# Performance work log

Measured on AMD Instinct MI355X. Metric: run time of the kernel, lower is better.

The kernel has to match this reference:

```python
import jax, jax.numpy as jnp
import numpy as np

TOP_K = 2

def setup_inputs() -> dict:
    key = jax.random.key(0)
    k0, k1, k2, k3 = jax.random.split(key, 4)
    B, T, D, F, E = 2, 2048, 1024, 4096, 8
    x = jax.random.normal(k0, (B, T, D), dtype=jnp.float32)
    Wr = jax.random.normal(k1, (E, D), dtype=jnp.float32) * 0.02   # router weight [out=E, in=D]
    W1 = jax.random.normal(k2, (E, F, D), dtype=jnp.float32) * 0.02  # per-expert up-proj [out=F, in=D]
    W2 = jax.random.normal(k3, (E, D, F), dtype=jnp.float32) * 0.02  # per-expert down-proj [out=D, in=F]
    return {"x": x, "Wr": Wr, "W1": W1, "W2": W2}

def reference(x, Wr, W1, W2):
    B, T, D = x.shape
    E = Wr.shape[0]
    N = B * T
    xf = x.reshape(N, D)
    # Router in fp32 on the un-cast activations (as in the torch module).
    logits = xf @ Wr.T                                   # [N, E]
    probs = jax.nn.softmax(logits, axis=-1)
    topk_w, topk_idx = jax.lax.top_k(probs, TOP_K)       # [N, K]
    topk_w = topk_w / jnp.sum(topk_w, axis=-1, keepdims=True)
    # Combine weights scattered into a dense [N, E] dispatch/combine matrix
    # (top_k indices are distinct, so .set is exact).
    combine = jnp.zeros((N, E), dtype=jnp.float32)
    combine = combine.at[jnp.arange(N)[:, None], topk_idx].set(topk_w)
    # Expert FFN runs in bf16 (comm_dtype in the original all-to-all pipeline).
    xb = xf.astype(jnp.bfloat16)
    h = jax.nn.gelu(jnp.einsum('nd,efd->enf', xb, W1.astype(jnp.bfloat16)),
                    approximate=False)                   # [E, N, F]
    yo = jnp.einsum('enf,edf->end', h, W2.astype(jnp.bfloat16))  # [E, N, D]
    # Weighted combine: bf16 expert outputs * fp32 gate weights -> fp32 (torch promotion).
    out = jnp.einsum('end,ne->nd', yo.astype(jnp.float32), combine)
    return out.reshape(B, T, D)
```

## Files before the change

### kernel.cpp

```cpp
#include <hip/hip_runtime.h>
#include <hip/hip_bf16.h>

typedef __attribute__((ext_vector_type(8))) __bf16 bf16x8;
typedef __attribute__((ext_vector_type(4))) float floatx4;

constexpr int N_TOK = 4096;
constexpr int DDIM  = 1024;
constexpr int FDIM  = 4096;
constexpr int NEXP  = 8;
constexpr int NSLOT = 2 * N_TOK;

static __device__ __forceinline__ unsigned short f2bf(float f) {
    union { __hip_bfloat16 h; unsigned short u; } v;
    v.h = __float2bfloat16(f);
    return v.u;
}

static __device__ __forceinline__ void gl2lds16(const unsigned short* g, unsigned short* l) {
    __builtin_amdgcn_global_load_lds(
        (__attribute__((address_space(1))) void*)g,
        (__attribute__((address_space(3))) void*)l,
        16, 0, 0);
}

__global__ void castX_kernel(const float* __restrict__ src, unsigned short* __restrict__ dst,
                             int* __restrict__ counts) {
    int i = blockIdx.x * 256 + threadIdx.x;
    float4 v = *(const float4*)(src + (size_t)i * 4);
    ushort4 o;
    o.x = f2bf(v.x); o.y = f2bf(v.y); o.z = f2bf(v.z); o.w = f2bf(v.w);
    *(ushort4*)(dst + (size_t)i * 4) = o;
    if (blockIdx.x == 0 && threadIdx.x < NEXP) counts[threadIdx.x] = 0;
}

__global__ void castN_kernel(const float* __restrict__ src, unsigned short* __restrict__ dst, int n4) {
    int i = blockIdx.x * 256 + threadIdx.x;
    if (i >= n4) return;
    float4 v = *(const float4*)(src + (size_t)i * 4);
    ushort4 o;
    o.x = f2bf(v.x); o.y = f2bf(v.y); o.z = f2bf(v.z); o.w = f2bf(v.w);
    *(ushort4*)(dst + (size_t)i * 4) = o;
}

__global__ void router_kernel(const float* __restrict__ x, const float* __restrict__ Wr,
                              int* __restrict__ te, float* __restrict__ tw,
                              int* __restrict__ counts) {
    __shared__ float wr[NEXP * DDIM];
    const int tid = threadIdx.x;
    for (int i = tid; i < NEXP * DDIM; i += 256) wr[i] = Wr[i];
    __syncthreads();
    const int wave = tid >> 6, lane = tid & 63;
    const int t = blockIdx.x * 4 + wave;

    float xr[16];
    const float* xp = x + (size_t)t * DDIM;
    #pragma unroll
    for (int i = 0; i < 16; i++) xr[i] = xp[lane + 64 * i];

    float logit[NEXP];
    #pragma unroll
    for (int e = 0; e < NEXP; e++) {
        float s = 0.f;
        #pragma unroll
        for (int i = 0; i < 16; i++) s += xr[i] * wr[e * DDIM + lane + 64 * i];
        #pragma unroll
        for (int off = 32; off > 0; off >>= 1) s += __shfl_xor(s, off, 64);
        logit[e] = s;
    }
    if (lane == 0) {
        int i0 = 0; float l0 = logit[0];
        #pragma unroll
        for (int e = 1; e < NEXP; e++) if (logit[e] > l0) { l0 = logit[e]; i0 = e; }
        int i1 = -1; float l1 = -3.0e38f;
        #pragma unroll
        for (int e = 0; e < NEXP; e++) if (e != i0 && logit[e] > l1) { l1 = logit[e]; i1 = e; }
        float p1 = expf(l1 - l0);
        float w0 = 1.f / (1.f + p1);
        float w1 = p1 * w0;
        te[t * 2] = i0; te[t * 2 + 1] = i1;
        tw[t * 2] = w0; tw[t * 2 + 1] = w1;
        atomicAdd(&counts[i0], 1);
        atomicAdd(&counts[i1], 1);
    }
}

__global__ void scan_kernel(const int* __restrict__ counts, int* __restrict__ offsets,
                            int* __restrict__ cursors) {
    if (threadIdx.x == 0) {
        int acc = 0;
        for (int e = 0; e < NEXP; e++) { offsets[e] = acc; acc += counts[e]; }
        offsets[NEXP] = acc;
    }
    if (threadIdx.x < NEXP) cursors[threadIdx.x] = 0;
}

__global__ void scatter_kernel(const int* __restrict__ te, const float* __restrict__ tw,
                               const int* __restrict__ offsets, int* __restrict__ cursors,
                               int* __restrict__ rowid, float* __restrict__ gate,
                               int* __restrict__ tok2slot) {
    int t = blockIdx.x * 256 + threadIdx.x;
    if (t >= N_TOK) return;
    #pragma unroll
    for (int k = 0; k < 2; k++) {
        int e = te[t * 2 + k];
        int pos = atomicAdd(&cursors[e], 1);
        int slot = offsets[e] + pos;
        rowid[slot] = t;
        gate[slot] = tw[t * 2 + k];
        tok2slot[t * 2 + k] = slot;
    }
}

template <int K, bool UP, bool BF16W>
__global__ __launch_bounds__(256)
void ffn_gemm(const unsigned short* __restrict__ A,
              const float* __restrict__ Wf,
              const unsigned short* __restrict__ Wb,
              unsigned short* __restrict__ Hout,
              float* __restrict__ Y,
              const int* __restrict__ rowid,
              const float* __restrict__ gate,
              const int* __restrict__ offsets) {
    constexpr int BM = 128, BN = 128, BK = 32, LDT = 32;
    constexpr int NOUT = UP ? FDIM : DDIM;

    const int e = blockIdx.z;
    const int seg = offsets[e];
    const int cnt = offsets[e + 1] - seg;
    const int m0 = blockIdx.y * BM;
    if (m0 >= cnt) return;
    const int n0 = blockIdx.x * BN;

    __shared__ __align__(16) unsigned short As[BM * LDT];
    __shared__ __align__(16) unsigned short Bs[BN * LDT];

    const int tid = threadIdx.x;
    const int lane = tid & 63;
    const int wave = tid >> 6;

    const int srow0 = wave * 32 + (lane >> 2);
    const int chunk = lane & 3;

    const unsigned short* ag[2];
    #pragma unroll
    for (int j = 0; j < 2; j++) {
        int r = srow0 + j * 16;
        int slot = seg + m0 + r;
        if (slot >= NSLOT) slot = NSLOT - 1;
        if (UP) { int t = rowid[slot]; ag[j] = A + (size_t)t * DDIM + chunk * 8; }
        else    { ag[j] = A + (size_t)slot * FDIM + chunk * 8; }
    }
    const unsigned short* bg[2];
    #pragma unroll
    for (int j = 0; j < 2; j++) {
        int r = srow0 + j * 16;
        bg[j] = Wb + ((size_t)e * NOUT + n0 + r) * K + chunk * 8;
    }
    unsigned short* asl[2];
    unsigned short* bsl[2];
    #pragma unroll
    for (int j = 0; j < 2; j++) {
        asl[j] = &As[(wave * 32 + j * 16) * LDT] + lane * 8;
        bsl[j] = &Bs[(wave * 32 + j * 16) * LDT] + lane * 8;
    }

    const int br = tid >> 1;
    const int bh = (tid & 1) * 16;
    const float* bptrf = Wf + ((size_t)e * NOUT + n0 + br) * K + bh;
    unsigned short* bsdst = &Bs[br * LDT + bh];

    const int wm = (wave >> 1) * 64;
    const int wn = (wave & 1) * 64;
    const int frow = lane & 15;
    const int quad = lane >> 4;

    floatx4 acc[4][4];
    #pragma unroll
    for (int i = 0; i < 4; i++)
        #pragma unroll
        for (int j = 0; j < 4; j++)
            acc[i][j] = (floatx4){0.f, 0.f, 0.f, 0.f};

    for (int k0 = 0; k0 < K; k0 += BK) {
        uint4 bu0, bu1;
        if (!BF16W) {
            float4 b0 = *(const float4*)(bptrf);
            float4 b1 = *(const float4*)(bptrf + 4);
            float4 b2 = *(const float4*)(bptrf + 8);
            float4 b3 = *(const float4*)(bptrf + 12);
            union { unsigned short u[16]; uint4 q[2]; } bb;
            bb.u[0] = f2bf(b0.x); bb.u[1] = f2bf(b0.y); bb.u[2]  = f2bf(b0.z); bb.u[3]  = f2bf(b0.w);
            bb.u[4] = f2bf(b1.x); bb.u[5] = f2bf(b1.y); bb.u[6]  = f2bf(b1.z); bb.u[7]  = f2bf(b1.w);
            bb.u[8] = f2bf(b2.x); bb.u[9] = f2bf(b2.y); bb.u[10] = f2bf(b2.z); bb.u[11] = f2bf(b2.w);
            bb.u[12] = f2bf(b3.x); bb.u[13] = f2bf(b3.y); bb.u[14] = f2bf(b3.z); bb.u[15] = f2bf(b3.w);
            bu0 = bb.q[0]; bu1 = bb.q[1];
            bptrf += BK;
        }
        __syncthreads();
        gl2lds16(ag[0], asl[0]);
        gl2lds16(ag[1], asl[1]);
        if (BF16W) {
            gl2lds16(bg[0], bsl[0]);
            gl2lds16(bg[1], bsl[1]);
            bg[0] += BK; bg[1] += BK;
        } else {
            *(uint4*)(bsdst) = bu0;
            *(uint4*)(bsdst + 8) = bu1;
        }
        ag[0] += BK; ag[1] += BK;
        __syncthreads();

        bf16x8 av[4], bv[4];
        #pragma unroll
        for (int i = 0; i < 4; i++)
            av[i] = *(const bf16x8*)&As[(wm + i * 16 + frow) * LDT + quad * 8];
        #pragma unroll
        for (int i = 0; i < 4; i++)
            bv[i] = *(const bf16x8*)&Bs[(wn + i * 16 + frow) * LDT + quad * 8];
        #pragma unroll
        for (int mt = 0; mt < 4; mt++)
            #pragma unroll
            for (int nt = 0; nt < 4; nt++)
                acc[mt][nt] = __builtin_amdgcn_mfma_f32_16x16x32_bf16(av[mt], bv[nt], acc[mt][nt], 0, 0, 0);
    }

    #pragma unroll
    for (int mt = 0; mt < 4; mt++) {
        #pragma unroll
        for (int r = 0; r < 4; r++) {
            int mloc = m0 + wm + mt * 16 + quad * 4 + r;
            if (mloc >= cnt) continue;
            int slot = seg + mloc;
            if (UP) {
                #pragma unroll
                for (int nt = 0; nt < 4; nt++) {
                    int n = n0 + wn + nt * 16 + frow;
                    float v = acc[mt][nt][r];
                    float g = 0.5f * v * (1.0f + erff(v * 0.70710678118654752f));
                    Hout[(size_t)slot * FDIM + n] = f2bf(g);
                }
            } else {
                float gw = gate[slot];
                #pragma unroll
                for (int nt = 0; nt < 4; nt++) {
                    int n = n0 + wn + nt * 16 + frow;
                    Y[(size_t)slot * DDIM + n] = gw * acc[mt][nt][r];
                }
            }
        }
    }
}

__global__ void combine_kernel(const float* __restrict__ Y, const int* __restrict__ tok2slot,
                               float* __restrict__ out) {
    int idx = blockIdx.x * 256 + threadIdx.x;
    int t = idx >> 8;
    int c = (idx & 255) * 4;
    int s0 = tok2slot[t * 2], s1 = tok2slot[t * 2 + 1];
    float4 a = *(const float4*)(Y + (size_t)s0 * DDIM + c);
    float4 b = *(const float4*)(Y + (size_t)s1 * DDIM + c);
    *(float4*)(out + (size_t)t * DDIM + c) =
        make_float4(a.x + b.x, a.y + b.y, a.z + b.z, a.w + b.w);
}

extern "C" void kernel_launch(void* const* d_in, const int* in_sizes, int n_in,
                              void* d_out, int out_size, void* d_ws, size_t ws_size,
                              hipStream_t stream) {
    const float* x  = (const float*)d_in[0];
    const float* Wr = (const float*)d_in[1];
    const float* W1 = (const float*)d_in[2];
    const float* W2 = (const float*)d_in[3];
    float* out = (float*)d_out;

    char* ws = (char*)d_ws;
    size_t off = 0;
    auto alloc = [&](size_t bytes) -> char* {
        char* p = ws + off;
        off = (off + bytes + 255) & ~(size_t)255;
        return p;
    };
    unsigned short* xb   = (unsigned short*)alloc((size_t)N_TOK * DDIM * 2);
    unsigned short* H    = (unsigned short*)alloc((size_t)NSLOT * FDIM * 2);
    float* Yb      = (float*)alloc((size_t)NSLOT * DDIM * 4);
    int*   rowid   = (int*)alloc(NSLOT * 4);
    float* gatew   = (float*)alloc(NSLOT * 4);
    int*   te      = (int*)alloc(NSLOT * 4);
    float* tw      = (float*)alloc(NSLOT * 4);
    int*   t2s     = (int*)alloc(NSLOT * 4);
    int*   counts  = (int*)alloc(64);
    int*   offsets = (int*)alloc(64);
    int*   cursors = (int*)alloc(64);
    unsigned short* w1b = (unsigned short*)alloc((size_t)NEXP * FDIM * DDIM * 2);
    unsigned short* w2b = (unsigned short*)alloc((size_t)NEXP * DDIM * FDIM * 2);
    const bool bf16w = (off <= ws_size);

    castX_kernel<<<N_TOK * DDIM / 4 / 256, 256, 0, stream>>>(x, xb, counts);
    if (bf16w) {
        const int n4 = NEXP * FDIM * DDIM / 4;
        castN_kernel<<<(n4 + 255) / 256, 256, 0, stream>>>(W1, w1b, n4);
        castN_kernel<<<(n4 + 255) / 256, 256, 0, stream>>>(W2, w2b, n4);
    }
    router_kernel<<<N_TOK / 4, 256, 0, stream>>>(x, Wr, te, tw, counts);
    scan_kernel<<<1, 64, 0, stream>>>(counts, offsets, cursors);
    scatter_kernel<<<(N_TOK + 255) / 256, 256, 0, stream>>>(te, tw, offsets, cursors, rowid, gatew, t2s);

    if (bf16w) {
        ffn_gemm<DDIM, true,  true ><<<dim3(FDIM / 128, 32, NEXP), 256, 0, stream>>>(xb, W1, w1b, H, Yb, rowid, gatew, offsets);
        ffn_gemm<FDIM, false, true ><<<dim3(DDIM / 128, 32, NEXP), 256, 0, stream>>>(H,  W2, w2b, H, Yb, rowid, gatew, offsets);
    } else {
        ffn_gemm<DDIM, true,  false><<<dim3(FDIM / 128, 32, NEXP), 256, 0, stream>>>(xb, W1, w1b, H, Yb, rowid, gatew, offsets);
        ffn_gemm<FDIM, false, false><<<dim3(DDIM / 128, 32, NEXP), 256, 0, stream>>>(H,  W2, w2b, H, Yb, rowid, gatew, offsets);
    }
    combine_kernel<<<N_TOK, 256, 0, stream>>>(Yb, t2s, out);
}
```

Baseline: 698.5 us.

## Schedule grouped GEMM over a compact per-expert tile list

The scan kernel now builds a compact list of (expert, m-tile) pairs, and the FFN GEMMs launch a 1D grid of MAXT times the n-tile count instead of a 3D grid padded to 32 m-tiles per expert. This removes the many empty early-exit blocks, and consecutive block IDs share the same n-tile, so weight tiles may be reused in L2 across m-tiles. The cost is a serial tile-list build in a single thread and an extra indirection per block. MAXT=72 assumes the tile count stays within that bound.

Result: no change. 711.5 us (+1.9%).

```diff
diff --git a/kernel.cpp b/kernel.cpp
--- a/kernel.cpp
+++ b/kernel.cpp
@@ -9,6 +9,7 @@
 constexpr int FDIM  = 4096;
 constexpr int NEXP  = 8;
 constexpr int NSLOT = 2 * N_TOK;
+constexpr int MAXT  = 72;
 
 static __device__ __forceinline__ unsigned short f2bf(float f) {
     union { __hip_bfloat16 h; unsigned short u; } v;
@@ -85,11 +86,19 @@
 }
 
 __global__ void scan_kernel(const int* __restrict__ counts, int* __restrict__ offsets,
-                            int* __restrict__ cursors) {
+                            int* __restrict__ cursors, int* __restrict__ tile_em,
+                            int* __restrict__ ntile) {
     if (threadIdx.x == 0) {
-        int acc = 0;
-        for (int e = 0; e < NEXP; e++) { offsets[e] = acc; acc += counts[e]; }
+        int acc = 0, nt = 0;
+        for (int e = 0; e < NEXP; e++) {
+            offsets[e] = acc;
+            for (int m0 = 0; m0 < counts[e]; m0 += 128)
+                tile_em[nt++] = (e << 16) | (m0 >> 7);
+            acc += counts[e];
+        }
         offsets[NEXP] = acc;
+        ntile[0] = nt;
+        for (int i = nt; i < MAXT; i++) tile_em[i] = 0;
     }
     if (threadIdx.x < NEXP) cursors[threadIdx.x] = 0;
 }
@@ -120,16 +129,20 @@
               float* __restrict__ Y,
               const int* __restrict__ rowid,
               const float* __restrict__ gate,
-              const int* __restrict__ offsets) {
+              const int* __restrict__ offsets,
+              const int* __restrict__ tile_em,
+              const int* __restrict__ ntile) {
     constexpr int BM = 128, BN = 128, BK = 32, LDT = 32;
     constexpr int NOUT = UP ? FDIM : DDIM;
 
-    const int e = blockIdx.z;
+    const int bt = blockIdx.x % MAXT;
+    if (bt >= ntile[0]) return;
+    const int em = tile_em[bt];
+    const int e  = em >> 16;
+    const int m0 = (em & 0xffff) << 7;
+    const int n0 = (blockIdx.x / MAXT) * BN;
     const int seg = offsets[e];
     const int cnt = offsets[e + 1] - seg;
-    const int m0 = blockIdx.y * BM;
-    if (m0 >= cnt) return;
-    const int n0 = blockIdx.x * BN;
 
     __shared__ __align__(16) unsigned short As[BM * LDT];
     __shared__ __align__(16) unsigned short Bs[BN * LDT];
@@ -290,6 +303,8 @@
     int*   counts  = (int*)alloc(64);
     int*   offsets = (int*)alloc(64);
     int*   cursors = (int*)alloc(64);
+    int*   tile_em = (int*)alloc(MAXT * 4);
+    int*   ntile   = (int*)alloc(64);
     unsigned short* w1b = (unsigned short*)alloc((size_t)NEXP * FDIM * DDIM * 2);
     unsigned short* w2b = (unsigned short*)alloc((size_t)NEXP * DDIM * FDIM * 2);
     const bool bf16w = (off <= ws_size);
@@ -301,15 +316,15 @@
         castN_kernel<<<(n4 + 255) / 256, 256, 0, stream>>>(W2, w2b, n4);
     }
     router_kernel<<<N_TOK / 4, 256, 0, stream>>>(x, Wr, te, tw, counts);
-    scan_kernel<<<1, 64, 0, stream>>>(counts, offsets, cursors);
+    scan_kernel<<<1, 64, 0, stream>>>(counts, offsets, cursors, tile_em, ntile);
     scatter_kernel<<<(N_TOK + 255) / 256, 256, 0, stream>>>(te, tw, offsets, cursors, rowid, gatew, t2s);
 
     if (bf16w) {
-        ffn_gemm<DDIM, true,  true ><<<dim3(FDIM / 128, 32, NEXP), 256, 0, stream>>>(xb, W1, w1b, H, Yb, rowid, gatew, offsets);
-        ffn_gemm<FDIM, false, true ><<<dim3(DDIM / 128, 32, NEXP), 256, 0, stream>>>(H,  W2, w2b, H, Yb, rowid, gatew, offsets);
+        ffn_gemm<DDIM, true,  true ><<<MAXT * (FDIM / 128), 256, 0, stream>>>(xb, W1, w1b, H, Yb, rowid, gatew, offsets, tile_em, ntile);
+        ffn_gemm<FDIM, false, true ><<<MAXT * (DDIM / 128), 256, 0, stream>>>(H,  W2, w2b, H, Yb, rowid, gatew, offsets, tile_em, ntile);
     } else {
-        ffn_gemm<DDIM, true,  false><<<dim3(FDIM / 128, 32, NEXP), 256, 0, stream>>>(xb, W1, w1b, H, Yb, rowid, gatew, offsets);
-        ffn_gemm<FDIM, false, false><<<dim3(DDIM / 128, 32, NEXP), 256, 0, stream>>>(H,  W2, w2b, H, Yb, rowid, gatew, offsets);
+        ffn_gemm<DDIM, true,  false><<<MAXT * (FDIM / 128), 256, 0, stream>>>(xb, W1, w1b, H, Yb, rowid, gatew, offsets, tile_em, ntile);
+        ffn_gemm<FDIM, false, false><<<MAXT * (DDIM / 128), 256, 0, stream>>>(H,  W2, w2b, H, Yb, rowid, gatew, offsets, tile_em, ntile);
     }
     combine_kernel<<<N_TOK, 256, 0, stream>>>(Yb, t2s, out);
 }
```
